# Performance work log

Hardware: AMD Instinct MI355X
Metric: run time of the kernel (lower is better)

## Reference

```python
import jax, jax.numpy as jnp
import numpy as np

D_MODEL = 1024
NUM_HEADS = 16
D_K = D_MODEL // NUM_HEADS


def setup_inputs() -> dict:
    key = jax.random.key(0)
    ks = jax.random.split(key, 7)
    B, S = 4, 2048
    lim = float(np.sqrt(6.0 / (D_MODEL + D_MODEL)))  # xavier uniform
    x = jax.random.normal(ks[0], (B, S, D_MODEL), dtype=jnp.float32)
    w_q = jax.random.uniform(ks[1], (D_MODEL, D_MODEL), jnp.float32, -lim, lim)
    w_k = jax.random.uniform(ks[2], (D_MODEL, D_MODEL), jnp.float32, -lim, lim)
    w_v = jax.random.uniform(ks[3], (D_MODEL, D_MODEL), jnp.float32, -lim, lim)
    w_o = jax.random.uniform(ks[4], (D_MODEL, D_MODEL), jnp.float32, -lim, lim)
    b_o = jnp.zeros((D_MODEL,), jnp.float32)
    ln_g = jnp.ones((D_MODEL,), jnp.float32)
    ln_b = jnp.zeros((D_MODEL,), jnp.float32)
    return {"x": x, "w_q": w_q, "w_k": w_k, "w_v": w_v, "w_o": w_o,
            "b_o": b_o, "ln_g": ln_g, "ln_b": ln_b}


def _layer_norm(y, g, b, eps=1e-5):
    mu = jnp.mean(y, axis=-1, keepdims=True)
    var = jnp.var(y, axis=-1, keepdims=True)
    return (y - mu) * jax.lax.rsqrt(var + eps) * g + b


def reference(x, w_q, w_k, w_v, w_o, b_o, ln_g, ln_b):
    B, S, D = x.shape
    # Linear weights stored torch-style [out, in]: y = x @ W^T
    def proj(w):
        return jnp.einsum('bsd,ed->bse', x, w).reshape(B, S, NUM_HEADS, D_K).transpose(0, 2, 1, 3)
    Q, K, V = proj(w_q), proj(w_k), proj(w_v)  # [B, H, S, d_k]
    scores = jnp.einsum('bhqd,bhkd->bhqk', Q, K) / jnp.sqrt(jnp.float32(D_K))
    attn = jax.nn.softmax(scores, axis=-1)  # dropout identity at eval
    out = jnp.einsum('bhqk,bhkd->bhqd', attn, V)  # [B, H, S, d_k]
    out = out.transpose(0, 2, 1, 3).reshape(B, S, D)
    out = jnp.einsum('bsd,ed->bse', out, w_o) + b_o
    return _layer_norm(x + out, ln_g, ln_b)
```

## Files before the change

### kernel.cpp

```cpp
#include <hip/hip_runtime.h>

typedef __bf16 bf16;
typedef bf16 v8bf __attribute__((ext_vector_type(8)));
typedef bf16 v4bf __attribute__((ext_vector_type(4)));
typedef float v4f __attribute__((ext_vector_type(4)));
typedef float v16f __attribute__((ext_vector_type(16)));
typedef unsigned int u32;
typedef u32 v4u __attribute__((ext_vector_type(4)));

#define GAS __attribute__((address_space(1)))
#define LAS __attribute__((address_space(3)))

constexpr int D    = 1024;
constexpr int ROWS = 8192;

__global__ __launch_bounds__(256) void cast_all(
    const float* __restrict__ x,
    const float* __restrict__ wq, const float* __restrict__ wk,
    const float* __restrict__ wv, const float* __restrict__ wo,
    bf16* __restrict__ xb, bf16* __restrict__ wqb, bf16* __restrict__ wkb,
    bf16* __restrict__ wvb, bf16* __restrict__ wob)
{
    int i = blockIdx.x * 256 + threadIdx.x;
    const float* src; bf16* dst; int off;
    if (i < 2 * 1024 * 1024) { src = x; dst = xb; off = i; }
    else {
        int j = i - 2 * 1024 * 1024;
        int w = j >> 18;
        off = j & ((1 << 18) - 1);
        src = (w == 0) ? wq : (w == 1) ? wk : (w == 2) ? wv : wo;
        dst = (w == 0) ? wqb : (w == 1) ? wkb : (w == 2) ? wvb : wob;
    }
    float4 v = ((const float4*)src)[off];
    v4bf o;
    o[0] = (bf16)v.x; o[1] = (bf16)v.y; o[2] = (bf16)v.z; o[3] = (bf16)v.w;
    ((v4bf*)dst)[off] = o;
}

template<int MODE, int NTN>
__global__ __launch_bounds__(512, 2) void gemm8(
    const bf16* __restrict__ A, const bf16* __restrict__ W,
    bf16* __restrict__ Oq, bf16* __restrict__ Ok, bf16* __restrict__ Ov,
    float* __restrict__ Of, const float* __restrict__ bias,
    const float* __restrict__ X)
{
    __shared__ bf16 Abuf[3][256 * 64];
    __shared__ bf16 Bbuf[3][128 * 64];

    const int id   = blockIdx.x;
    const int wgid = (id & 7) * (4 * NTN) + (id >> 3);
    const int mT   = wgid / NTN;
    const int nT   = wgid - mT * NTN;
    const long rowA0 = (long)mT * 256;
    const long colB0 = (long)nT * 128;

    const int tid  = threadIdx.x;
    const int lane = tid & 63;
    const int wave = tid >> 6;
    const int quad = lane >> 4;
    const int l16  = lane & 15;
    const int wm   = (wave >> 1) * 64;
    const int wn   = (wave & 1) * 64;

    const int srow = wave * 8 + (lane >> 3);
    const int scol = ((lane & 7) ^ (lane >> 3)) * 8;
    const bf16* gA = A + (rowA0 + srow) * D + scol;
    const bf16* gB = W + (colB0 + srow) * D + scol;
    const int dstOff = wave * 512;

    const v4f vzero = {0.f, 0.f, 0.f, 0.f};
    v4f acc[4][4];
    #pragma unroll
    for (int i = 0; i < 4; i++)
        #pragma unroll
        for (int j = 0; j < 4; j++) acc[i][j] = vzero;

    int sa[2], sb[2];
    #pragma unroll
    for (int ks = 0; ks < 2; ks++) {
        const int ch = ((ks * 4 + quad) ^ (l16 & 7)) * 8;
        sa[ks] = (wm + l16) * 64 + ch;
        sb[ks] = (wn + l16) * 64 + ch;
    }

    auto stage_full = [&](int bi, int t) {
        const bf16* a = gA + (long)t * 64;
        const bf16* b = gB + (long)t * 64;
        #pragma unroll
        for (int i = 0; i < 4; i++)
            __builtin_amdgcn_global_load_lds(
                (const GAS void*)(a + (long)i * 64 * D),
                (LAS void*)(&Abuf[bi][i * 4096 + dstOff]), 16, 0, 0);
        #pragma unroll
        for (int i = 0; i < 2; i++)
            __builtin_amdgcn_global_load_lds(
                (const GAS void*)(b + (long)i * 64 * D),
                (LAS void*)(&Bbuf[bi][i * 4096 + dstOff]), 16, 0, 0);
    };

    constexpr int NT = 16;
    stage_full(0, 0);
    stage_full(1, 1);
    asm volatile("s_waitcnt vmcnt(6)" ::: "memory");
    __builtin_amdgcn_s_barrier();

    for (int t = 0; t < NT; ++t) {
        const int bi = t % 3;
        const int bs = (t + 2) % 3;
        const bf16* As = &Abuf[bi][0];
        const bf16* Bs = &Bbuf[bi][0];
        #pragma unroll
        for (int ks = 0; ks < 2; ++ks) {
            v8bf af[4], bf4[4];
            #pragma unroll
            for (int mi = 0; mi < 4; mi++)
                af[mi] = *(const v8bf*)(As + sa[ks] + mi * 1024);
            #pragma unroll
            for (int ni = 0; ni < 4; ni++)
                bf4[ni] = *(const v8bf*)(Bs + sb[ks] + ni * 1024);

            if (t + 2 < NT) {
                const bf16* a2 = gA + (long)(t + 2) * 64;
                const bf16* b2 = gB + (long)(t + 2) * 64;
                if (ks == 0) {
                    __builtin_amdgcn_global_load_lds(
                        (const GAS void*)(a2),
                        (LAS void*)(&Abuf[bs][dstOff]), 16, 0, 0);
                    __builtin_amdgcn_global_load_lds(
                        (const GAS void*)(a2 + (long)64 * D),
                        (LAS void*)(&Abuf[bs][4096 + dstOff]), 16, 0, 0);
                    __builtin_amdgcn_global_load_lds(
                        (const GAS void*)(b2),
                        (LAS void*)(&Bbuf[bs][dstOff]), 16, 0, 0);
                } else {
                    __builtin_amdgcn_global_load_lds(
                        (const GAS void*)(a2 + (long)128 * D),
                        (LAS void*)(&Abuf[bs][2 * 4096 + dstOff]), 16, 0, 0);
                    __builtin_amdgcn_global_load_lds(
                        (const GAS void*)(a2 + (long)192 * D),
                        (LAS void*)(&Abuf[bs][3 * 4096 + dstOff]), 16, 0, 0);
                    __builtin_amdgcn_global_load_lds(
                        (const GAS void*)(b2 + (long)64 * D),
                        (LAS void*)(&Bbuf[bs][4096 + dstOff]), 16, 0, 0);
                }
            }

            if (ks == 1 && t + 1 < NT) {
                if (t + 2 < NT) asm volatile("s_waitcnt vmcnt(6)" ::: "memory");
                else            asm volatile("s_waitcnt vmcnt(0)" ::: "memory");
            }

            __builtin_amdgcn_s_barrier();
            asm volatile("s_waitcnt lgkmcnt(0)" ::: "memory");
            __builtin_amdgcn_sched_barrier(0);
            __builtin_amdgcn_s_setprio(1);
            #pragma unroll
            for (int mi = 0; mi < 4; mi++)
                #pragma unroll
                for (int ni = 0; ni < 4; ni++)
                    acc[mi][ni] = __builtin_amdgcn_mfma_f32_16x16x32_bf16(
                        af[mi], bf4[ni], acc[mi][ni], 0, 0, 0);
            __builtin_amdgcn_s_setprio(0);
            __builtin_amdgcn_s_barrier();
        }
    }

    const float qscale = 0.125f * 1.44269504f;

    if (MODE == 0) {
        const int z = (int)(colB0 >> 10);
        #pragma unroll
        for (int mi = 0; mi < 4; mi++) {
            #pragma unroll
            for (int ni = 0; ni < 4; ni++) {
                const long col = colB0 + wn + ni * 16 + l16;
                const long c   = col & 1023;
                const long row0 = rowA0 + wm + mi * 16 + quad * 4;
                if (z == 2) {
                    const long h_ = c >> 6, dd = c & 63;
                    const long b_ = row0 >> 11, s0 = row0 & 2047;
                    v4bf pk;
                    #pragma unroll
                    for (int r = 0; r < 4; r++) pk[r] = (bf16)acc[mi][ni][r];
                    *(v4bf*)(Ov + ((b_ * 16 + h_) * 64 + dd) * 2048 + s0) = pk;
                } else {
                    bf16* Ob = (z == 0) ? Oq : Ok;
                    #pragma unroll
                    for (int r = 0; r < 4; r++) {
                        float v = acc[mi][ni][r];
                        if (z == 0) v *= qscale;
                        Ob[(row0 + r) * D + c] = (bf16)v;
                    }
                }
            }
        }
    } else {
        #pragma unroll
        for (int mi = 0; mi < 4; mi++) {
            #pragma unroll
            for (int ni = 0; ni < 4; ni++) {
                const long col = colB0 + wn + ni * 16 + l16;
                const float bv = bias[col];
                #pragma unroll
                for (int r = 0; r < 4; r++) {
                    const long row = rowA0 + wm + mi * 16 + quad * 4 + r;
                    Of[row * D + col] = acc[mi][ni][r] + bv + X[row * D + col];
                }
            }
        }
    }
}

__global__ __launch_bounds__(512, 4) void attn_kernel(
    const bf16* __restrict__ Q, const bf16* __restrict__ Kg,
    const bf16* __restrict__ VtG, bf16* __restrict__ O)
{
    const int id  = blockIdx.x;
    const int xcd = id & 7, j = id >> 3;
    const int qt  = j & 7;
    const int g   = xcd + 8 * (j >> 3);
    const int h   = g & 15, b = g >> 4;

    const int tid  = threadIdx.x;
    const int lane = tid & 63;
    const int wave = tid >> 6;
    const int l31  = lane & 31;
    const int hi   = lane >> 5;

    __shared__ bf16 Kt[4][64 * 64];
    __shared__ bf16 Vt[4][64 * 64];

    const long qrow = (long)(b * 2048 + qt * 256 + wave * 32 + l31);
    v8bf qB[4];
    #pragma unroll
    for (int f = 0; f < 4; f++)
        qB[f] = *(const v8bf*)(Q + qrow * D + h * 64 + f * 16 + hi * 8);

    const v16f z16 = {0.f,0.f,0.f,0.f,0.f,0.f,0.f,0.f,
                      0.f,0.f,0.f,0.f,0.f,0.f,0.f,0.f};
    v16f o_acc[2];
    o_acc[0] = z16; o_acc[1] = z16;
    float l0 = 0.f, l1 = 0.f;

    const int iR = tid >> 3;
    const int c8 = tid & 7;
    const bf16* kLane = Kg  + (long)b * 2048 * D + h * 64 + c8 * 8 + (long)iR * D;
    const bf16* vLane = VtG + (long)(b * 16 + h) * 64 * 2048 + c8 * 8 + (long)iR * 2048;
    const int wOff = iR * 64 + ((c8 ^ (iR & 7)) * 8);

    v8bf kp[2], vp[2];
    kp[0] = *(const v8bf*)(kLane); vp[0] = *(const v8bf*)(vLane);
    kLane += 64 * D; vLane += 64;
    kp[1] = *(const v8bf*)(kLane); vp[1] = *(const v8bf*)(vLane);
    kLane += 64 * D; vLane += 64;
    *(v8bf*)(&Kt[0][wOff]) = kp[0]; *(v8bf*)(&Vt[0][wOff]) = vp[0];
    *(v8bf*)(&Kt[1][wOff]) = kp[1]; *(v8bf*)(&Vt[1][wOff]) = vp[1];
    kp[0] = *(const v8bf*)(kLane); vp[0] = *(const v8bf*)(vLane);
    kLane += 64 * D; vLane += 64;
    kp[1] = *(const v8bf*)(kLane); vp[1] = *(const v8bf*)(vLane);
    kLane += 64 * D; vLane += 64;

    auto compute = [&](const int bq) {
        #pragma unroll
        for (int ko = 0; ko < 2; ko++) {
            const int krow = ko * 32 + l31;
            const int ksw  = krow & 7;
            v8bf kA[4];
            #pragma unroll
            for (int f = 0; f < 4; f++)
                kA[f] = *(const v8bf*)(&Kt[bq][krow * 64 + (((2 * f + hi) ^ ksw) * 8)]);
            __builtin_amdgcn_s_setprio(1);
            v16f st = __builtin_amdgcn_mfma_f32_32x32x16_bf16(kA[0], qB[0], z16, 0, 0, 0);
            st = __builtin_amdgcn_mfma_f32_32x32x16_bf16(kA[1], qB[1], st, 0, 0, 0);
            st = __builtin_amdgcn_mfma_f32_32x32x16_bf16(kA[2], qB[2], st, 0, 0, 0);
            st = __builtin_amdgcn_mfma_f32_32x32x16_bf16(kA[3], qB[3], st, 0, 0, 0);
            __builtin_amdgcn_s_setprio(0);

            float p[16];
            #pragma unroll
            for (int r = 0; r < 16; r++) {
                p[r] = __builtin_amdgcn_exp2f(st[r]);
                if (r & 1) l1 += p[r]; else l0 += p[r];
            }

            #pragma unroll
            for (int u = 0; u < 2; u++) {
                const int s = ko * 2 + u;
                u32 a0, a1, b0, b1;
                asm("v_cvt_pk_bf16_f32 %0, %1, %2" : "=v"(a0) : "v"(p[u*8+0]), "v"(p[u*8+1]));
                asm("v_cvt_pk_bf16_f32 %0, %1, %2" : "=v"(a1) : "v"(p[u*8+2]), "v"(p[u*8+3]));
                asm("v_cvt_pk_bf16_f32 %0, %1, %2" : "=v"(b0) : "v"(p[u*8+4]), "v"(p[u*8+5]));
                asm("v_cvt_pk_bf16_f32 %0, %1, %2" : "=v"(b1) : "v"(p[u*8+6]), "v"(p[u*8+7]));
                asm("v_permlane32_swap_b32 %0, %1" : "+v"(a0), "+v"(b0));
                asm("v_permlane32_swap_b32 %0, %1" : "+v"(a1), "+v"(b1));
                v4u w; w[0] = a0; w[1] = a1; w[2] = b0; w[3] = b1;
                const v8bf pa = __builtin_bit_cast(v8bf, w);
                const int vsw = (l31 & 7);
                v8bf vb0 = *(const v8bf*)(&Vt[bq][(l31)      * 64 + (((2 * s + hi) ^ vsw) * 8)]);
                v8bf vb1 = *(const v8bf*)(&Vt[bq][(32 + l31) * 64 + (((2 * s + hi) ^ vsw) * 8)]);
                __builtin_amdgcn_s_setprio(1);
                o_acc[0] = __builtin_amdgcn_mfma_f32_32x32x16_bf16(pa, vb0, o_acc[0], 0, 0, 0);
                o_acc[1] = __builtin_amdgcn_mfma_f32_32x32x16_bf16(pa, vb1, o_acc[1], 0, 0, 0);
                __builtin_amdgcn_s_setprio(0);
            }
        }
    };

    for (int gg = 0; gg < 16; ++gg) {
        const int cb = (gg & 1) * 2;
        __syncthreads();

        if (gg < 15) {
            *(v8bf*)(&Kt[cb ^ 2][wOff])       = kp[0];
            *(v8bf*)(&Vt[cb ^ 2][wOff])       = vp[0];
            *(v8bf*)(&Kt[(cb ^ 2) + 1][wOff]) = kp[1];
            *(v8bf*)(&Vt[(cb ^ 2) + 1][wOff]) = vp[1];
        }
        if (gg < 14) {
            kp[0] = *(const v8bf*)(kLane); vp[0] = *(const v8bf*)(vLane);
            kLane += 64 * D; vLane += 64;
            kp[1] = *(const v8bf*)(kLane); vp[1] = *(const v8bf*)(vLane);
            kLane += 64 * D; vLane += 64;
        }

        compute(cb);
        compute(cb + 1);
    }

    float l_acc = l0 + l1;
    l_acc += __shfl_xor(l_acc, 32);

    const long obase = (long)(b * 2048 + qt * 256 + wave * 32);
    #pragma unroll
    for (int r = 0; r < 16; r++) {
        const int qp = (r & 3) + 8 * (r >> 2) + 4 * hi;
        const float inv = 1.f / __shfl(l_acc, qp);
        O[(obase + qp) * D + h * 64 + l31]      = (bf16)(o_acc[0][r] * inv);
        O[(obase + qp) * D + h * 64 + 32 + l31] = (bf16)(o_acc[1][r] * inv);
    }
}

__global__ __launch_bounds__(256) void ln_kernel(
    const float* __restrict__ g, const float* __restrict__ beta,
    float* __restrict__ out)
{
    const int row = blockIdx.x;
    const int t = threadIdx.x;
    const int lane = t & 63, wave = t >> 6;
    const long base = (long)row * D + t * 4;

    float4 yv = *(const float4*)(out + base);
    float y0 = yv.x, y1 = yv.y, y2 = yv.z, y3 = yv.w;
    float s1 = y0 + y1 + y2 + y3;
    float s2 = y0*y0 + y1*y1 + y2*y2 + y3*y3;
    #pragma unroll
    for (int off = 1; off < 64; off <<= 1) {
        s1 += __shfl_xor(s1, off);
        s2 += __shfl_xor(s2, off);
    }
    __shared__ float r1[4], r2[4];
    if (lane == 0) { r1[wave] = s1; r2[wave] = s2; }
    __syncthreads();
    float S1 = r1[0] + r1[1] + r1[2] + r1[3];
    float S2 = r2[0] + r2[1] + r2[2] + r2[3];
    float mu  = S1 * (1.f / 1024.f);
    float var = S2 * (1.f / 1024.f) - mu * mu;
    float rsd = rsqrtf(var + 1e-5f);

    float4 gv = *(const float4*)(g + t * 4);
    float4 bv = *(const float4*)(beta + t * 4);
    float4 o;
    o.x = (y0 - mu) * rsd * gv.x + bv.x;
    o.y = (y1 - mu) * rsd * gv.y + bv.y;
    o.z = (y2 - mu) * rsd * gv.z + bv.z;
    o.w = (y3 - mu) * rsd * gv.w + bv.w;
    *(float4*)(out + base) = o;
}

extern "C" void kernel_launch(void* const* d_in, const int* in_sizes, int n_in,
                              void* d_out, int out_size, void* d_ws, size_t ws_size,
                              hipStream_t stream)
{
    const float* x   = (const float*)d_in[0];
    const float* wq  = (const float*)d_in[1];
    const float* wk  = (const float*)d_in[2];
    const float* wv  = (const float*)d_in[3];
    const float* wo  = (const float*)d_in[4];
    const float* bo  = (const float*)d_in[5];
    const float* lng = (const float*)d_in[6];
    const float* lnb = (const float*)d_in[7];
    float* out = (float*)d_out;

    char* ws = (char*)d_ws;
    bf16* xb  = (bf16*)(ws);
    bf16* wqb = (bf16*)(ws + (size_t)16 * 1024 * 1024);
    bf16* wkb = wqb + 1024 * 1024;
    bf16* wvb = wkb + 1024 * 1024;
    bf16* wob = wvb + 1024 * 1024;
    bf16* Qb  = (bf16*)(ws + (size_t)24 * 1024 * 1024);
    bf16* Kb  = Qb + (size_t)ROWS * D;
    bf16* VtG = Kb + (size_t)ROWS * D;
    bf16* Ab  = VtG + (size_t)ROWS * D;

    cast_all<<<12288, 256, 0, stream>>>(x, wq, wk, wv, wo,
                                        xb, wqb, wkb, wvb, wob);

    gemm8<0, 24><<<768, 512, 0, stream>>>(xb, wqb, Qb, Kb, VtG,
                                          nullptr, nullptr, nullptr);

    attn_kernel<<<dim3(512, 1, 1), 512, 0, stream>>>(Qb, Kb, VtG, Ab);

    gemm8<1, 8><<<256, 512, 0, stream>>>(Ab, wob, nullptr, nullptr, nullptr,
                                         out, bo, x);

    ln_kernel<<<8192, 256, 0, stream>>>(lng, lnb, out);
}
```

Before: 278.6 us.

## Stage K/V tiles via direct global-to-LDS loads in a triple-buffered pipeline

Replaces register-staged K/V loads and LDS stores with global_load_lds DMA writes directly into shared memory. The source column is pre-swizzled so the existing XOR layout is preserved. A three-slot ring with one barrier per 64-key tile replaces the double-pair buffering, and launch bounds drop from 4 to 2 blocks per CU. This removes VGPR staging and ds_write instructions, but the lower occupancy hint and the finer per-tile barrier cadence could reduce latency hiding.

```diff
diff --git a/kernel.cpp b/kernel.cpp
--- a/kernel.cpp
+++ b/kernel.cpp
@@ -211,7 +211,7 @@
     }
 }
 
-__global__ __launch_bounds__(512, 4) void attn_kernel(
+__global__ __launch_bounds__(512, 2) void attn_kernel(
     const bf16* __restrict__ Q, const bf16* __restrict__ Kg,
     const bf16* __restrict__ VtG, bf16* __restrict__ O)
 {
@@ -227,8 +227,8 @@
     const int l31  = lane & 31;
     const int hi   = lane >> 5;
 
-    __shared__ bf16 Kt[4][64 * 64];
-    __shared__ bf16 Vt[4][64 * 64];
+    __shared__ bf16 Kt[3][64 * 64];
+    __shared__ bf16 Vt[3][64 * 64];
 
     const long qrow = (long)(b * 2048 + qt * 256 + wave * 32 + l31);
     v8bf qB[4];
@@ -242,23 +242,21 @@
     o_acc[0] = z16; o_acc[1] = z16;
     float l0 = 0.f, l1 = 0.f;
 
-    const int iR = tid >> 3;
-    const int c8 = tid & 7;
-    const bf16* kLane = Kg  + (long)b * 2048 * D + h * 64 + c8 * 8 + (long)iR * D;
-    const bf16* vLane = VtG + (long)(b * 16 + h) * 64 * 2048 + c8 * 8 + (long)iR * 2048;
-    const int wOff = iR * 64 + ((c8 ^ (iR & 7)) * 8);
-
-    v8bf kp[2], vp[2];
-    kp[0] = *(const v8bf*)(kLane); vp[0] = *(const v8bf*)(vLane);
-    kLane += 64 * D; vLane += 64;
-    kp[1] = *(const v8bf*)(kLane); vp[1] = *(const v8bf*)(vLane);
-    kLane += 64 * D; vLane += 64;
-    *(v8bf*)(&Kt[0][wOff]) = kp[0]; *(v8bf*)(&Vt[0][wOff]) = vp[0];
-    *(v8bf*)(&Kt[1][wOff]) = kp[1]; *(v8bf*)(&Vt[1][wOff]) = vp[1];
-    kp[0] = *(const v8bf*)(kLane); vp[0] = *(const v8bf*)(vLane);
-    kLane += 64 * D; vLane += 64;
-    kp[1] = *(const v8bf*)(kLane); vp[1] = *(const v8bf*)(vLane);
-    kLane += 64 * D; vLane += 64;
+    const int iR  = tid >> 3;
+    const int c8  = tid & 7;
+    const int csw = ((c8 ^ (iR & 7)) * 8);
+    const bf16* kSrc = Kg  + (long)b * 2048 * D + h * 64 + csw + (long)iR * D;
+    const bf16* vSrc = VtG + (long)(b * 16 + h) * 64 * 2048 + csw + (long)iR * 2048;
+    const int ldsOff = wave * 512;
+
+    auto stage = [&](int bi, int t) {
+        __builtin_amdgcn_global_load_lds(
+            (const GAS void*)(kSrc + (long)t * 64 * D),
+            (LAS void*)(&Kt[bi][ldsOff]), 16, 0, 0);
+        __builtin_amdgcn_global_load_lds(
+            (const GAS void*)(vSrc + t * 64),
+            (LAS void*)(&Vt[bi][ldsOff]), 16, 0, 0);
+    };
 
     auto compute = [&](const int bq) {
         #pragma unroll
@@ -306,25 +304,20 @@
         }
     };
 
-    for (int gg = 0; gg < 16; ++gg) {
-        const int cb = (gg & 1) * 2;
-        __syncthreads();
-
-        if (gg < 15) {
-            *(v8bf*)(&Kt[cb ^ 2][wOff])       = kp[0];
-            *(v8bf*)(&Vt[cb ^ 2][wOff])       = vp[0];
-            *(v8bf*)(&Kt[(cb ^ 2) + 1][wOff]) = kp[1];
-            *(v8bf*)(&Vt[(cb ^ 2) + 1][wOff]) = vp[1];
+    stage(0, 0);
+    stage(1, 1);
+    asm volatile("s_waitcnt vmcnt(2)" ::: "memory");
+    __builtin_amdgcn_s_barrier();
+
+    for (int kt = 0; kt < 32; ++kt) {
+        const int bi = kt % 3;
+        if (kt + 2 < 32) stage((kt + 2) % 3, kt + 2);
+        compute(bi);
+        if (kt + 1 < 32) {
+            if (kt + 2 < 32) asm volatile("s_waitcnt vmcnt(2)" ::: "memory");
+            else             asm volatile("s_waitcnt vmcnt(0)" ::: "memory");
+            __builtin_amdgcn_s_barrier();
         }
-        if (gg < 14) {
-            kp[0] = *(const v8bf*)(kLane); vp[0] = *(const v8bf*)(vLane);
-            kLane += 64 * D; vLane += 64;
-            kp[1] = *(const v8bf*)(kLane); vp[1] = *(const v8bf*)(vLane);
-            kLane += 64 * D; vLane += 64;
-        }
-
-        compute(cb);
-        compute(cb + 1);
     }
 
     float l_acc = l0 + l1;
```

Result: no change. 278.2 us (-0.1%).
